# Optimization experiments

Measured on AMD Instinct MI355X. Metric: run time of the kernel, lower is better.

Reference implementation:

```python
import jax, jax.numpy as jnp
import numpy as np
from jax import lax

# --- constants from init_kwargs ---
B, N = 1, 6
C_IN, MID, C_CTX, D = 512, 512, 80, 112
OGH, OGW = 256, 704
DSF = 16
FH, FW = OGH // DSF, OGW // DSF  # 16, 44
D_MIN, D_MAX = 2.0, 58.0
NX, NY, NZ = 128, 128, 1
VOXEL_SIZE = np.array([0.8, 0.8, 8.0], np.float32)
VOXEL_COORD = np.array([-51.2 + 0.4, -51.2 + 0.4, -5.0 + 4.0], np.float32)
VOXEL_NUM = np.array([NX, NY, NZ], np.int32)


def _conv(x, w, b=None):
    pad = (w.shape[-1] - 1) // 2
    y = lax.conv_general_dilated(x, w, (1, 1), [(pad, pad), (pad, pad)],
                                 dimension_numbers=('NCHW', 'OIHW', 'NCHW'))
    if b is not None:
        y = y + b[None, :, None, None]
    return y


def _depthnet(x, w_s1, w_s2, w_d1, w_d2, b_d, w_c1, w_c2, b_c):
    # BatchNorm layers at init (gamma=1, beta=0, running stats 0/1) are identity in eval
    x = jax.nn.relu(_conv(x, w_s1))
    x = jax.nn.relu(_conv(x, w_s2))
    depth_logits = _conv(jax.nn.relu(_conv(x, w_d1)), w_d2, b_d)   # [BN, D, FH, FW]
    context = _conv(jax.nn.relu(_conv(x, w_c1)), w_c2, b_c)        # [BN, C_CTX, FH, FW]
    return depth_logits, context


def _frustum():
    d = jnp.linspace(D_MIN, D_MAX, D, dtype=jnp.float32)            # [D]
    u = jnp.linspace(0.0, OGW - 1.0, FW, dtype=jnp.float32)         # [FW]
    v = jnp.linspace(0.0, OGH - 1.0, FH, dtype=jnp.float32)         # [FH]
    uu = jnp.broadcast_to(u[None, None, :], (D, FH, FW))
    vv = jnp.broadcast_to(v[None, :, None], (D, FH, FW))
    uv1 = jnp.stack([uu, vv, jnp.ones_like(uu)], axis=-1)           # [D,FH,FW,3]
    return uv1, d


def _geometry(sensor2ego, intrin, ida, bda):
    uv1, d = _frustum()
    ida_inv = jnp.linalg.inv(ida)                                   # [B,N,4,4]
    R_ida, t_ida = ida_inv[..., :3, :3], ida_inv[..., :3, 3]
    uv1_pre = jnp.einsum('bnij,dhwj->bndhwi', R_ida, uv1) + t_ida[:, :, None, None, None, :]
    K_inv = jnp.linalg.inv(intrin[..., :3, :3])
    rays = jnp.einsum('bnij,bndhwj->bndhwi', K_inv, uv1_pre)
    pts_cam = rays * d[None, None, :, None, None, None]             # [B,N,D,FH,FW,3]
    pts4 = jnp.concatenate([pts_cam, jnp.ones_like(pts_cam[..., :1])], axis=-1)
    pts_ego = jnp.einsum('bnij,bndhwj->bndhwi', sensor2ego, pts4)
    pts_ego = jnp.einsum('bij,bndhwj->bndhwi', bda, pts_ego)
    return pts_ego[..., :3]                                         # [B,N,D,FH,FW,3]


def _voxel_pooling(geom_xyz, feats):
    # geom_xyz: [B,N,D,FH,FW,3] int32 voxel coords; feats: [B,N,D,FH,FW,C]
    C = feats.shape[-1]
    g = geom_xyz.reshape(B, -1, 3)                                  # [B,M,3]
    valid = jnp.all((g >= 0) & (g < jnp.asarray(VOXEL_NUM)[None, None, :]), axis=-1)
    idx = g[..., 1] * NX + g[..., 0]                                # y*nx + x (z collapsed, NZ=1)
    idx = idx + jnp.arange(B, dtype=jnp.int32)[:, None] * (NY * NX)
    idx = jnp.where(valid, idx, B * NY * NX)                        # dump bucket
    f = feats.reshape(B * g.shape[1], C)
    out = jax.ops.segment_sum(f, idx.reshape(-1), num_segments=B * NY * NX + 1)
    out = out[:B * NY * NX].reshape(B, NY, NX, C)
    return jnp.transpose(out, (0, 3, 1, 2))                         # [B,C,NY,NX]


def setup_inputs() -> dict:
    key = jax.random.key(0)
    ks = jax.random.split(key, 8)

    def w(k, shape):
        fan_in = shape[1] * shape[2] * shape[3]
        return jax.random.normal(k, shape, jnp.float32) * np.sqrt(2.0 / fan_in)

    inp = {
        'source_features': jax.random.normal(ks[0], (B * N, C_IN, FH, FW), jnp.float32),
        'w_s1': w(ks[1], (MID, C_IN, 3, 3)),
        'w_s2': w(ks[2], (MID, MID, 3, 3)),
        'w_d1': w(ks[3], (MID, MID, 3, 3)),
        'w_d2': w(ks[4], (D, MID, 1, 1)),
        'b_d': jnp.zeros((D,), jnp.float32),
        'w_c1': w(ks[5], (MID, MID, 3, 3)),
        'w_c2': w(ks[6], (C_CTX, MID, 1, 1)),
        'b_c': jnp.zeros((C_CTX,), jnp.float32),
    }

    # realistic camera rig: 6 cameras yawed around ego, cam-forward (z) -> ego-forward
    base = np.array([[0., 0., 1.], [-1., 0., 0.], [0., -1., 0.]], np.float32)
    s2e = np.zeros((B, N, 4, 4), np.float32)
    for n in range(N):
        yaw = 2.0 * np.pi * n / N
        c, s = np.cos(yaw), np.sin(yaw)
        Rz = np.array([[c, -s, 0.], [s, c, 0.], [0., 0., 1.]], np.float32)
        s2e[0, n, :3, :3] = Rz @ base
        s2e[0, n, :3, 3] = [0.0, 0.0, 1.5]
        s2e[0, n, 3, 3] = 1.0
    intrin = np.zeros((B, N, 4, 4), np.float32)
    intrin[:, :] = np.eye(4, dtype=np.float32)
    intrin[:, :, 0, 0] = 560.0
    intrin[:, :, 1, 1] = 560.0
    intrin[:, :, 0, 2] = OGW / 2.0
    intrin[:, :, 1, 2] = OGH / 2.0
    ida = np.broadcast_to(np.eye(4, dtype=np.float32), (B, N, 4, 4)).copy()
    bda = np.broadcast_to(np.eye(4, dtype=np.float32), (B, 4, 4)).copy()

    inp['sensor2ego_mats'] = jnp.asarray(s2e)
    inp['intrin_mats'] = jnp.asarray(intrin)
    inp['ida_mats'] = jnp.asarray(ida)
    inp['bda_mat'] = jnp.asarray(bda)
    return inp


def reference(source_features, w_s1, w_s2, w_d1, w_d2, b_d, w_c1, w_c2, b_c,
              sensor2ego_mats, intrin_mats, ida_mats, bda_mat):
    depth_logits, context = _depthnet(source_features, w_s1, w_s2, w_d1, w_d2, b_d, w_c1, w_c2, b_c)
    depth_prob = jax.nn.softmax(depth_logits, axis=1)               # [BN,D,FH,FW]
    # depth-weighted context: [BN, C, D, FH, FW]
    feat = depth_prob[:, None, :, :, :] * context[:, :, None, :, :]
    feat = feat.reshape(B, N, C_CTX, D, FH, FW).transpose(0, 1, 3, 4, 5, 2)  # [B,N,D,FH,FW,C]
    pts_ego = _geometry(sensor2ego_mats, intrin_mats, ida_mats, bda_mat)
    vs = jnp.asarray(VOXEL_SIZE)
    vc = jnp.asarray(VOXEL_COORD)
    geom_xyz = ((pts_ego - (vc - vs / 2.0)) / vs).astype(jnp.int32)
    return _voxel_pooling(geom_xyz, feat)                            # [B,C,NY,NX]
```

## Files before the change

### kernel.cpp

```cpp
#include <hip/hip_runtime.h>


#define FH_ 16
#define FW_ 44
#define SP_ 704
#define XSTR 960
#define NIMG 6
#define CIN 512
#define DCH 112
#define CCTX 80
#define NXY 128
#define NVOX (NXY * NXY)
#define NPTS (NIMG * DCH * SP_)
#define CHUNK 64

#define NKC7 8
#define HCHK 360448
#define CIP 40

typedef unsigned short u16;
typedef unsigned int u32;
typedef __attribute__((ext_vector_type(8))) short bf16x8;
typedef __attribute__((ext_vector_type(4))) short s16x4;
typedef __attribute__((ext_vector_type(4))) float f32x4;
typedef __attribute__((ext_vector_type(16))) float f32x16;

__device__ __forceinline__ float bf2f(u16 b) {
    union { unsigned u; float f; } v; v.u = ((unsigned)b) << 16; return v.f;
}
__device__ __forceinline__ u16 f2bf(float f) {
    union { float f; unsigned u; } v; v.f = f;
    unsigned r = v.u + 0x7fffu + ((v.u >> 16) & 1u);
    return (u16)(r >> 16);
}
__device__ __forceinline__ int spad_of(int s) {
    return (s / 44) * 46 + (s % 44) + 47;
}
__device__ __forceinline__ void gld_lds16(const void* gsrc, void* ldst) {
    __builtin_amdgcn_global_load_lds(
        (const __attribute__((address_space(1))) u32*)gsrc,
        (__attribute__((address_space(3))) u32*)ldst, 16, 0, 0);
}
__device__ __forceinline__ _Float16* chunk6(_Float16* pA, _Float16* pB, int q, int n) {
    int c = q * 6 + n;
    return (c < 6) ? (pA + (size_t)c * HCHK) : (pB + (size_t)(c - 6) * HCHK);
}

__global__ void zero_k(float4* __restrict__ p, long n4) {
    long i = (long)blockIdx.x * blockDim.x + threadIdx.x;
    if (i < n4) p[i] = make_float4(0.f, 0.f, 0.f, 0.f);
}

__global__ void src_to_xt_k(const float* __restrict__ src, short* __restrict__ xt) {
    int e = blockIdx.x * 256 + threadIdx.x;
    if (e >= NIMG * SP_ * CIN) return;
    int ci = e & 511;
    int r = e >> 9;
    int s = r % SP_, n = r / SP_;
    float v = src[((size_t)n * CIN + ci) * SP_ + s];
    xt[(((size_t)n * 32 + (ci >> 4)) * XSTR + spad_of(s)) * 16 + (ci & 15)] = (short)f2bf(v);
}

__global__ void wsplit2_k(const float* __restrict__ wA, short* __restrict__ oA,
                          const float* __restrict__ wB, short* __restrict__ oB) {
    int i = blockIdx.x * 256 + threadIdx.x;
    if (i >= 2 * CIN * CIN) return;
    const int e = i & (CIN * CIN - 1);
    const float* __restrict__ w = (i < CIN * CIN) ? wA : wB;
    short* __restrict__ o = (i < CIN * CIN) ? oA : oB;
    const int co = e >> 9, ci = e & 511;
    const float* wp = w + (size_t)e * 9;
#pragma unroll
    for (int t = 0; t < 9; ++t)
        o[((((size_t)(ci >> 4) * 9) + t) * CIN + co) * 16 + (ci & 15)] = (short)f2bf(wp[t]);
}

__global__ void wsplit1_dual_k(const float* __restrict__ wd, short* __restrict__ od,
                               const float* __restrict__ wc, short* __restrict__ oc) {
    int i = blockIdx.x * 256 + threadIdx.x;
    if (i < DCH * CIN) od[i] = (short)f2bf(wd[i]);
    else if (i < DCH * CIN + CCTX * CIN) {
        int j = i - DCH * CIN;
        oc[j] = (short)f2bf(wc[j]);
    }
}

__global__ __launch_bounds__(128, 2) void conv7_k(
    const short* __restrict__ xt2, const short* __restrict__ w2,
    _Float16* __restrict__ pA, _Float16* __restrict__ pB)
{
    __shared__ short Xs[2][256 * 16];
    __shared__ short Wsh[2][576 * 16];
    const int tid = threadIdx.x;
    const int lane = tid & 63, wave = tid >> 6;
    const int l31 = lane & 31, lh = lane >> 5;

    const int bid = blockIdx.x;
    const int c32 = bid & 31;
    const int cb = c32 >> 2, q = c32 & 3;
    const int rest = bid >> 5;
    const int n = rest / 6, sb = rest - (rest / 6) * 6;

    const int s0 = sb * 128;
    const int co0 = cb * 64;
    const int base = spad_of(s0) - 47;

    const short* __restrict__ xq = xt2 + (((size_t)n * 32 + q * 8) * XSTR + base) * 16;
    const short* __restrict__ wq = w2 + (((size_t)(q * 8) * 9) * CIN + co0) * 16;

    int sloc[2];
#pragma unroll
    for (int mf = 0; mf < 2; ++mf)
        sloc[mf] = spad_of(s0 + wave * 64 + mf * 32 + l31) - base;

    const f32x16 z16 = {0.f,0.f,0.f,0.f,0.f,0.f,0.f,0.f,
                        0.f,0.f,0.f,0.f,0.f,0.f,0.f,0.f};
    f32x16 acc[2][2];
    acc[0][0] = z16; acc[0][1] = z16; acc[1][0] = z16; acc[1][1] = z16;

#define STAGE7(BUF, KC) do {                                                    \
    const short* xc = xq + (size_t)(KC) * (XSTR * 16) + lane * 8;               \
    const short* wc = wq + (size_t)(KC) * (9 * CIN * 16) + lane * 8;            \
    _Pragma("unroll")                                                           \
    for (int i = 0; i < 13; ++i) {                                              \
        const int sg = wave + 2 * i;                                            \
        if (sg < 8) {                                                           \
            gld_lds16(xc + sg * 512, &Xs[BUF][sg * 512]);                       \
        } else {                                                                \
            const int j = sg - 8;                                               \
            gld_lds16(wc + (j >> 1) * (CIN * 16) + (j & 1) * 512,               \
                      &Wsh[BUF][j * 512]);                                      \
        }                                                                       \
    }                                                                           \
} while (0)

    STAGE7(0, 0);
    __syncthreads();

    constexpr int OFF[9] = {-47, -46, -45, -1, 0, 1, 45, 46, 47};
    for (int kc = 0; kc < NKC7; ++kc) {
        if (kc + 1 < NKC7) STAGE7((kc + 1) & 1, kc + 1);
        const short* __restrict__ Xb = Xs[kc & 1];
        const short* __restrict__ Wb = Wsh[kc & 1];
#pragma unroll
        for (int t9 = 0; t9 < 9; ++t9) {
            const int off = OFF[t9];
            bf16x8 a0 = *(const bf16x8*)&Xb[(sloc[0] + off) * 16 + lh * 8];
            bf16x8 a1 = *(const bf16x8*)&Xb[(sloc[1] + off) * 16 + lh * 8];
            bf16x8 b0 = *(const bf16x8*)&Wb[(t9 * 64 + l31) * 16 + lh * 8];
            bf16x8 b1 = *(const bf16x8*)&Wb[(t9 * 64 + 32 + l31) * 16 + lh * 8];
            acc[0][0] = __builtin_amdgcn_mfma_f32_32x32x16_bf16(a0, b0, acc[0][0], 0, 0, 0);
            acc[0][1] = __builtin_amdgcn_mfma_f32_32x32x16_bf16(a0, b1, acc[0][1], 0, 0, 0);
            acc[1][0] = __builtin_amdgcn_mfma_f32_32x32x16_bf16(a1, b0, acc[1][0], 0, 0, 0);
            acc[1][1] = __builtin_amdgcn_mfma_f32_32x32x16_bf16(a1, b1, acc[1][1], 0, 0, 0);
        }
        __syncthreads();
    }
#undef STAGE7

    _Float16* __restrict__ Pc = chunk6(pA, pB, q, n);
#pragma unroll
    for (int mf = 0; mf < 2; ++mf) {
        const int spb = wave * 64 + mf * 32 + 4 * lh;
#pragma unroll
        for (int r = 0; r < 16; ++r) {
            const int sg = s0 + spb + (r & 3) + 8 * (r >> 2);
            if (sg < SP_) {
                const size_t ro = (size_t)sg * 512 + co0 + l31;
                Pc[ro] = (_Float16)acc[mf][0][r];
                Pc[ro + 32] = (_Float16)acc[mf][1][r];
            }
        }
    }
}

__global__ __launch_bounds__(256) void combine6_k(
    _Float16* __restrict__ pA, _Float16* __restrict__ pB, short* __restrict__ xout)
{
    const int i = blockIdx.x * 256 + threadIdx.x;
    if (i >= NIMG * SP_ * CIN / 4) return;
    const int e = i * 4;
    const int n = e / (SP_ * CIN);
    const int r = e - n * (SP_ * CIN);
    const int s = r >> 9, co = r & 511;
    union h4 { s16x4 s; _Float16 h[4]; };
    float v[4] = {0.f, 0.f, 0.f, 0.f};
#pragma unroll
    for (int q = 0; q < 4; ++q) {
        const _Float16* c = chunk6(pA, pB, q, n);
        h4 u; u.s = *(const s16x4*)(c + r);
#pragma unroll
        for (int j = 0; j < 4; ++j) v[j] += (float)u.h[j];
    }
    s16x4 o;
#pragma unroll
    for (int j = 0; j < 4; ++j) o[j] = (short)f2bf(fmaxf(v[j], 0.f));
    *(s16x4*)&xout[(((size_t)n * 32 + (co >> 4)) * XSTR + spad_of(s)) * 16 + (co & 15)] = o;
}

__global__ __launch_bounds__(256, 2) void gemm1x1d_k(
    const short* __restrict__ xA, const short* __restrict__ wA,
    const float* __restrict__ bA, float* __restrict__ oA,
    const short* __restrict__ xB, const short* __restrict__ wB,
    const float* __restrict__ bB, float* __restrict__ oB)
{
    const int sel = blockIdx.y;
    const short* __restrict__ xtin = sel ? xB : xA;
    const short* __restrict__ wb   = sel ? wB : wA;
    const float* __restrict__ bias = sel ? bB : bA;
    float* __restrict__ outT       = sel ? oB : oA;
    const int nst = sel ? (CCTX / 16) : (DCH / 16);
    const int nco = nst * 16;

    __shared__ short Wb[DCH * CIP];
    const int tid = threadIdx.x;
    const int s0 = blockIdx.x * 128, n = blockIdx.z;
    const int lane = tid & 63, wave = tid >> 6;
    const int kg = lane >> 4, lrow = lane & 15;
    const int swave = s0 + wave * 32;

    int arow[2];
#pragma unroll
    for (int ms = 0; ms < 2; ++ms)
        arow[ms] = spad_of(swave + ms * 16 + lrow);

    const f32x4 zero4 = {0.f, 0.f, 0.f, 0.f};
    f32x4 acc[2][7];
#pragma unroll
    for (int ms = 0; ms < 2; ++ms)
#pragma unroll
        for (int ns = 0; ns < 7; ++ns) acc[ms][ns] = zero4;

    const short* xb = xtin + (size_t)n * 32 * XSTR * 16;

    for (int kc = 0; kc < 16; ++kc) {
        __syncthreads();
#pragma unroll
        for (int it = 0; it < 2; ++it) {
            int q = it * 256 + tid;
            if (q < nco * 4) {
                int co = q >> 2, p = q & 3;
                *(bf16x8*)&Wb[co * CIP + p * 8] =
                    *(const bf16x8*)(wb + (size_t)co * CIN + kc * 32 + p * 8);
            }
        }
        __syncthreads();
        bf16x8 a[2];
#pragma unroll
        for (int ms = 0; ms < 2; ++ms) {
            const int kcc = 2 * kc + (kg >> 1);
            a[ms] = *(const bf16x8*)(xb + ((size_t)kcc * XSTR + arow[ms]) * 16 + (kg & 1) * 8);
        }
#pragma unroll
        for (int ns = 0; ns < 7; ++ns) {
            if (ns < nst) {
                int co = ns * 16 + lrow;
                bf16x8 b = *(const bf16x8*)&Wb[co * CIP + kg * 8];
#pragma unroll
                for (int ms = 0; ms < 2; ++ms)
                    acc[ms][ns] = __builtin_amdgcn_mfma_f32_16x16x32_bf16(
                        a[ms], b, acc[ms][ns], 0, 0, 0);
            }
        }
    }
#pragma unroll
    for (int ms = 0; ms < 2; ++ms)
#pragma unroll
        for (int ns = 0; ns < 7; ++ns) {
            if (ns < nst) {
#pragma unroll
                for (int r = 0; r < 4; ++r) {
                    int sg = swave + ms * 16 + kg * 4 + r;
                    if (sg < SP_) {
                        int co = ns * 16 + lrow;
                        outT[((size_t)n * SP_ + sg) * nco + co] = acc[ms][ns][r] + bias[co];
                    }
                }
            }
        }
}

__global__ __launch_bounds__(256) void softmax2_k(
    const float* __restrict__ lg, float* __restrict__ pr)
{
    const int p = blockIdx.x * 4 + (threadIdx.x >> 6);
    if (p >= NIMG * SP_) return;
    const int lane = threadIdx.x & 63;
    const float* lp = lg + (size_t)p * DCH;
    float v0 = lp[lane];
    float v1 = (lane < DCH - 64) ? lp[64 + lane] : -1e30f;
    float m = fmaxf(v0, v1);
#pragma unroll
    for (int o = 32; o; o >>= 1) m = fmaxf(m, __shfl_xor(m, o));
    float e0 = __expf(v0 - m);
    float e1 = (lane < DCH - 64) ? __expf(v1 - m) : 0.f;
    float s = e0 + e1;
#pragma unroll
    for (int o = 32; o; o >>= 1) s += __shfl_xor(s, o);
    const float inv = 1.f / s;
    float* pp = pr + (size_t)p * DCH;
    pp[lane] = e0 * inv;
    if (lane < DCH - 64) pp[64 + lane] = e1 * inv;
}

__device__ __forceinline__ void inv4(const double* M, double* inv) {
    inv[0]  =  M[5]*M[10]*M[15] - M[5]*M[11]*M[14] - M[9]*M[6]*M[15] + M[9]*M[7]*M[14] + M[13]*M[6]*M[11] - M[13]*M[7]*M[10];
    inv[4]  = -M[4]*M[10]*M[15] + M[4]*M[11]*M[14] + M[8]*M[6]*M[15] - M[8]*M[7]*M[14] - M[12]*M[6]*M[11] + M[12]*M[7]*M[10];
    inv[8]  =  M[4]*M[9]*M[15]  - M[4]*M[11]*M[13] - M[8]*M[5]*M[15] + M[8]*M[7]*M[13] + M[12]*M[5]*M[11] - M[12]*M[7]*M[9];
    inv[12] = -M[4]*M[9]*M[14]  + M[4]*M[10]*M[13] + M[8]*M[5]*M[14] - M[8]*M[6]*M[13] - M[12]*M[5]*M[10] + M[12]*M[6]*M[9];
    inv[1]  = -M[1]*M[10]*M[15] + M[1]*M[11]*M[14] + M[9]*M[2]*M[15] - M[9]*M[3]*M[14] - M[13]*M[2]*M[11] + M[13]*M[3]*M[10];
    inv[5]  =  M[0]*M[10]*M[15] - M[0]*M[11]*M[14] - M[8]*M[2]*M[15] + M[8]*M[3]*M[14] + M[12]*M[2]*M[11] - M[12]*M[3]*M[10];
    inv[9]  = -M[0]*M[9]*M[15]  + M[0]*M[11]*M[13] + M[8]*M[1]*M[15] - M[8]*M[3]*M[13] - M[12]*M[1]*M[11] + M[12]*M[3]*M[9];
    inv[13] =  M[0]*M[9]*M[14]  - M[0]*M[10]*M[13] - M[8]*M[1]*M[14] + M[8]*M[2]*M[13] + M[12]*M[1]*M[10] - M[12]*M[2]*M[9];
    inv[2]  =  M[1]*M[6]*M[15]  - M[1]*M[7]*M[14]  - M[5]*M[2]*M[15] + M[5]*M[3]*M[14] + M[13]*M[2]*M[7]  - M[13]*M[3]*M[6];
    inv[6]  = -M[0]*M[6]*M[15]  + M[0]*M[7]*M[14]  + M[4]*M[2]*M[15] - M[4]*M[3]*M[14] - M[12]*M[2]*M[7]  + M[12]*M[3]*M[6];
    inv[10] =  M[0]*M[5]*M[15]  - M[0]*M[7]*M[13]  - M[4]*M[1]*M[15] + M[4]*M[3]*M[13] + M[12]*M[1]*M[7]  - M[12]*M[3]*M[5];
    inv[14] = -M[0]*M[5]*M[14]  + M[0]*M[6]*M[13]  + M[4]*M[1]*M[14] - M[4]*M[2]*M[13] - M[12]*M[1]*M[6]  + M[12]*M[2]*M[5];
    inv[3]  = -M[1]*M[6]*M[11]  + M[1]*M[7]*M[10]  + M[5]*M[2]*M[11] - M[5]*M[3]*M[10] - M[9]*M[2]*M[7]   + M[9]*M[3]*M[6];
    inv[7]  =  M[0]*M[6]*M[11]  - M[0]*M[7]*M[10]  - M[4]*M[2]*M[11] + M[4]*M[3]*M[10] + M[8]*M[2]*M[7]   - M[8]*M[3]*M[6];
    inv[11] = -M[0]*M[5]*M[11]  + M[0]*M[7]*M[9]   + M[4]*M[1]*M[11] - M[4]*M[3]*M[9]  - M[8]*M[1]*M[7]   + M[8]*M[3]*M[5];
    inv[15] =  M[0]*M[5]*M[10]  - M[0]*M[6]*M[9]   - M[4]*M[1]*M[10] + M[4]*M[2]*M[9]  + M[8]*M[1]*M[6]   - M[8]*M[2]*M[5];
    double det = M[0]*inv[0] + M[1]*inv[4] + M[2]*inv[8] + M[3]*inv[12];
    double id = 1.0 / det;
#pragma unroll
    for (int i = 0; i < 16; ++i) inv[i] *= id;
}

__global__ void geom_setup_k(const float* __restrict__ s2e, const float* __restrict__ intrin,
                             const float* __restrict__ ida, const float* __restrict__ bda,
                             double* __restrict__ gc)
{
    const int n = threadIdx.x;
    if (n >= NIMG) return;
    double M[16], Iv[16];
#pragma unroll
    for (int i = 0; i < 16; ++i) M[i] = (double)ida[n * 16 + i];
    inv4(M, Iv);
    double R[3][3], tv[3];
#pragma unroll
    for (int r = 0; r < 3; ++r) {
#pragma unroll
        for (int c = 0; c < 3; ++c) R[r][c] = Iv[r * 4 + c];
        tv[r] = Iv[r * 4 + 3];
    }
    double K[3][3];
#pragma unroll
    for (int r = 0; r < 3; ++r)
#pragma unroll
        for (int c = 0; c < 3; ++c) K[r][c] = (double)intrin[n * 16 + r * 4 + c];
    double det = K[0][0] * (K[1][1] * K[2][2] - K[1][2] * K[2][1])
               - K[0][1] * (K[1][0] * K[2][2] - K[1][2] * K[2][0])
               + K[0][2] * (K[1][0] * K[2][1] - K[1][1] * K[2][0]);
    double id = 1.0 / det;
    double Ki[3][3];
    Ki[0][0] = (K[1][1] * K[2][2] - K[1][2] * K[2][1]) * id;
    Ki[0][1] = (K[0][2] * K[2][1] - K[0][1] * K[2][2]) * id;
    Ki[0][2] = (K[0][1] * K[1][2] - K[0][2] * K[1][1]) * id;
    Ki[1][0] = (K[1][2] * K[2][0] - K[1][0] * K[2][2]) * id;
    Ki[1][1] = (K[0][0] * K[2][2] - K[0][2] * K[2][0]) * id;
    Ki[1][2] = (K[0][2] * K[1][0] - K[0][0] * K[1][2]) * id;
    Ki[2][0] = (K[1][0] * K[2][1] - K[1][1] * K[2][0]) * id;
    Ki[2][1] = (K[0][1] * K[2][0] - K[0][0] * K[2][1]) * id;
    Ki[2][2] = (K[0][0] * K[1][1] - K[0][1] * K[1][0]) * id;
    double A[3][3], bv[3];
#pragma unroll
    for (int r = 0; r < 3; ++r) {
#pragma unroll
        for (int c = 0; c < 3; ++c)
            A[r][c] = Ki[r][0] * R[0][c] + Ki[r][1] * R[1][c] + Ki[r][2] * R[2][c];
        bv[r] = Ki[r][0] * tv[0] + Ki[r][1] * tv[1] + Ki[r][2] * tv[2];
    }
    double* g = gc + n * 24;
#pragma unroll
    for (int r = 0; r < 3; ++r)
#pragma unroll
        for (int c = 0; c < 3; ++c) g[r * 3 + c] = A[r][c];
#pragma unroll
    for (int r = 0; r < 3; ++r) g[9 + r] = bv[r];
#pragma unroll
    for (int r = 0; r < 3; ++r)
#pragma unroll
        for (int c = 0; c < 4; ++c) {
            double acc = 0.0;
#pragma unroll
            for (int k = 0; k < 4; ++k)
                acc += (double)bda[r * 4 + k] * (double)s2e[n * 16 + k * 4 + c];
            g[12 + r * 4 + c] = acc;
        }
}

__global__ __launch_bounds__(256) void point_voxel_k(
    const double* __restrict__ gc, int* __restrict__ vidx, int* __restrict__ cnt)
{
    const int i = blockIdx.x * 256 + threadIdx.x;
    if (i >= NPTS) return;
    const int lane = threadIdx.x & 63;
    const int n = i / (DCH * SP_);
    int r = i - n * (DCH * SP_);
    const int di = r / SP_;
    const int s = r - di * SP_;
    const int h = s / FW_, w = s - h * FW_;
    const double* g = gc + n * 24;
    const double u  = (double)(float)((double)w * (703.0 / 43.0));
    const double v  = (double)(float)((double)h * 17.0);
    const double dd = (double)(float)(2.0 + (double)di * (56.0 / 111.0));
    const double rx = g[0] * u + g[1] * v + g[2] + g[9];
    const double ry = g[3] * u + g[4] * v + g[5] + g[10];
    const double rz = g[6] * u + g[7] * v + g[8] + g[11];
    const double px = rx * dd, py = ry * dd, pz = rz * dd;
    const double ex = g[12] * px + g[13] * py + g[14] * pz + g[15];
    const double ey = g[16] * px + g[17] * py + g[18] * pz + g[19];
    const double ez = g[20] * px + g[21] * py + g[22] * pz + g[23];
    const double vs_xy = 0.8, vs_z = 8.0;
    const double offx = (double)(float)(-51.2 + 0.4) - vs_xy * 0.5;
    const double offz = (double)(float)(-5.0 + 4.0) - vs_z * 0.5;
    const int gx = (int)((ex - offx) / vs_xy);
    const int gy = (int)((ey - offx) / vs_xy);
    const int gz = (int)((ez - offz) / vs_z);
    const bool ok = (gx >= 0 && gx < NXY && gy >= 0 && gy < NXY && gz == 0);
    const int vv = ok ? (gy * NXY + gx) : -1;
    vidx[i] = vv;
    unsigned long long unresolved = __ballot(vv >= 0);
    while (unresolved) {
        const int src = __ffsll(unresolved) - 1;
        const int v0 = __shfl(vv, src);
        const unsigned long long grp = __ballot(vv == v0);
        if (lane == src) atomicAdd(&cnt[v0], __popcll(grp));
        unresolved &= ~grp;
    }
}

__global__ void prefix_k(const int* __restrict__ cnt, int* __restrict__ off,
                         int* __restrict__ cur) {
    __shared__ int part[256];
    const int t = threadIdx.x;
    int s = 0;
    for (int j = 0; j < 64; ++j) s += cnt[t * 64 + j];
    part[t] = s;
    __syncthreads();
    if (t == 0) {
        int run = 0;
        for (int k = 0; k < 256; ++k) { int v = part[k]; part[k] = run; run += v; }
    }
    __syncthreads();
    int base = part[t];
    for (int j = 0; j < 64; ++j) {
        off[t * 64 + j] = base;
        cur[t * 64 + j] = base;
        base += cnt[t * 64 + j];
    }
    if (t == 255) off[NVOX] = base;
}

__global__ __launch_bounds__(256) void fill_k(
    const int* __restrict__ vidx, const float* __restrict__ prob,
    int* __restrict__ cur, int2* __restrict__ pk) {
    int i = blockIdx.x * 256 + threadIdx.x;
    if (i >= NPTS) return;
    const int lane = threadIdx.x & 63;
    const int v = vidx[i];
    const int n = i / (DCH * SP_);
    int r = i - n * (DCH * SP_);
    const int di = r / SP_;
    const int s = r - di * SP_;
    float p = 0.f;
    if (v >= 0) p = prob[((size_t)n * SP_ + s) * DCH + di];

    int pos = -1;
    unsigned long long unresolved = __ballot(v >= 0);
    while (unresolved) {
        const int src = __ffsll(unresolved) - 1;
        const int v0 = __shfl(v, src);
        const unsigned long long grp = __ballot(v == v0);
        int base = 0;
        if (lane == src) base = atomicAdd(&cur[v0], __popcll(grp));
        base = __shfl(base, src);
        if (v == v0) {
            const int rank = __popcll(grp & ((1ull << lane) - 1ull));
            pos = base + rank;
        }
        unresolved &= ~grp;
    }
    if (v >= 0)
        pk[pos] = make_int2((v << 13) | (n * SP_ + s), __float_as_int(p));
}

__global__ __launch_bounds__(256) void gather2_k(
    const int2* __restrict__ pk, const int* __restrict__ off,
    const float* __restrict__ ctxT, float* __restrict__ accT)
{
    const int gtid = blockIdx.x * 256 + threadIdx.x;
    const int wid = gtid >> 6;
    const int lane = threadIdx.x & 63;
    const int total = off[NVOX];
    const int lo = wid * CHUNK;
    if (lo >= total) return;
    const int hi = min(lo + CHUNK, total);
    float a0 = 0.f, a1 = 0.f;
    int2 e = pk[lo];
    for (int k = lo; k < hi; ++k) {
        const int2 en = (k + 1 < hi) ? pk[k + 1] : make_int2(-1, 0);
        const float p = __int_as_float(e.y);
        const int ns = e.x & 8191;
        const float* cb = ctxT + (size_t)ns * CCTX;
        a0 = fmaf(p, cb[lane], a0);
        if (lane < CCTX - 64) a1 = fmaf(p, cb[64 + lane], a1);
        if ((en.x >> 13) != (e.x >> 13)) {
            float* ab = accT + (size_t)(e.x >> 13) * CCTX;
            atomicAdd(ab + lane, a0);
            if (lane < CCTX - 64) atomicAdd(ab + 64 + lane, a1);
            a0 = a1 = 0.f;
        }
        e = en;
    }
}

__global__ void transpose_out_k(const float* __restrict__ accT, float* __restrict__ out) {
    const int idx = blockIdx.x * 256 + threadIdx.x;
    if (idx >= CCTX * NVOX) return;
    const int c = idx >> 14;
    const int v = idx & 16383;
    out[idx] = accT[(size_t)v * CCTX + c];
}

#define O_WHIA  512
#define O_WHIB  1180160
#define O_XT0   2359808
#define O_XT1   3834368
#define O_XT2   5308928
#define O_WD2B  6783488
#define O_WC2B  6812160
#define O_DLG   6832640
#define O_DPR   7305728
#define O_CTX   7778816
#define O_PK    8116736
#define O_VIX   9062912
#define O_CNT   9536000
#define O_OFF   9552384
#define O_CUR   9568784
#define O_ACC   9585168

extern "C" void kernel_launch(void* const* d_in, const int* in_sizes, int n_in,
                              void* d_out, int out_size, void* d_ws, size_t ws_size,
                              hipStream_t stream)
{
    const float* src  = (const float*)d_in[0];
    const float* w_s1 = (const float*)d_in[1];
    const float* w_s2 = (const float*)d_in[2];
    const float* w_d1 = (const float*)d_in[3];
    const float* w_d2 = (const float*)d_in[4];
    const float* b_d  = (const float*)d_in[5];
    const float* w_c1 = (const float*)d_in[6];
    const float* w_c2 = (const float*)d_in[7];
    const float* b_c  = (const float*)d_in[8];
    const float* s2e  = (const float*)d_in[9];
    const float* intr = (const float*)d_in[10];
    const float* ida  = (const float*)d_in[11];
    const float* bda  = (const float*)d_in[12];

    double* gc = (double*)d_ws;
    float* ws   = (float*)d_ws;
    short* whiA = (short*)(ws + O_WHIA);
    short* whiC = (short*)(ws + O_XT2);
    _Float16* pA = (_Float16*)(ws + O_WHIB);
    _Float16* pB = (_Float16*)(ws + O_WD2B);
    short* xt0  = (short*)(ws + O_XT0);
    short* xt1  = (short*)(ws + O_XT1);
    short* xt2  = (short*)(ws + O_XT2);
    short* wd2b = (short*)(ws + O_WD2B);
    short* wc2b = (short*)(ws + O_WC2B);
    float* dlog = ws + O_DLG;
    float* dprb = ws + O_DPR;
    float* ctxT = ws + O_CTX;
    int2*  pk   = (int2*)(ws + O_PK);
    int* vidx   = (int*)(ws + O_VIX);
    int* cnt    = (int*)(ws + O_CNT);
    int* offs   = (int*)(ws + O_OFF);
    int* cur    = (int*)(ws + O_CUR);
    float* accT = ws + O_ACC;
    float* out  = (float*)d_out;

    const int CMB = (NIMG * SP_ * CIN / 4 + 255) / 256;

    zero_k<<<(2949120 / 4 + 255) / 256, 256, 0, stream>>>((float4*)xt0, 2949120 / 4);

    geom_setup_k<<<1, 64, 0, stream>>>(s2e, intr, ida, bda, gc);
    src_to_xt_k<<<(NIMG * SP_ * CIN + 255) / 256, 256, 0, stream>>>(src, xt0);

    wsplit2_k<<<(2 * CIN * CIN) / 256, 256, 0, stream>>>(w_s1, whiA, w_s2, whiC);
    conv7_k<<<1152, 128, 0, stream>>>(xt0, whiA, pA, pB);
    combine6_k<<<CMB, 256, 0, stream>>>(pA, pB, xt1);
    conv7_k<<<1152, 128, 0, stream>>>(xt1, whiC, pA, pB);
    combine6_k<<<CMB, 256, 0, stream>>>(pA, pB, xt0);
    wsplit2_k<<<(2 * CIN * CIN) / 256, 256, 0, stream>>>(w_c1, whiA, w_d1, whiC);
    conv7_k<<<1152, 128, 0, stream>>>(xt0, whiA, pA, pB);
    combine6_k<<<CMB, 256, 0, stream>>>(pA, pB, xt1);
    conv7_k<<<1152, 128, 0, stream>>>(xt0, whiC, pA, pB);
    combine6_k<<<CMB, 256, 0, stream>>>(pA, pB, xt2);

    wsplit1_dual_k<<<((DCH + CCTX) * CIN + 255) / 256, 256, 0, stream>>>(w_d2, wd2b, w_c2, wc2b);
    gemm1x1d_k<<<dim3(6, 2, NIMG), 256, 0, stream>>>(xt2, wd2b, b_d, dlog,
                                                     xt1, wc2b, b_c, ctxT);
    softmax2_k<<<(NIMG * SP_ + 3) / 4, 256, 0, stream>>>(dlog, dprb);

    zero_k<<<(NVOX / 4 + 255) / 256, 256, 0, stream>>>((float4*)cnt, NVOX / 4);
    point_voxel_k<<<(NPTS + 255) / 256, 256, 0, stream>>>(gc, vidx, cnt);
    prefix_k<<<1, 256, 0, stream>>>(cnt, offs, cur);
    fill_k<<<(NPTS + 255) / 256, 256, 0, stream>>>(vidx, dprb, cur, pk);

    zero_k<<<(1310720 / 4 + 255) / 256, 256, 0, stream>>>((float4*)accT, 1310720 / 4);
    {
        const int waves = (NPTS + CHUNK - 1) / CHUNK;
        const int blocks = (waves + 3) / 4;
        gather2_k<<<blocks, 256, 0, stream>>>(pk, offs, ctxT, accT);
    }
    transpose_out_k<<<(CCTX * NVOX + 255) / 256, 256, 0, stream>>>(accT, out);

    (void)in_sizes; (void)n_in; (void)out_size; (void)ws_size;
}
```

Before: 421.4 us.

## Widen conv tile to 128 output channels and load weights directly from global

```diff
diff --git a/kernel.cpp b/kernel.cpp
--- a/kernel.cpp
+++ b/kernel.cpp
@@ -14,7 +14,7 @@
 #define NPTS (NIMG * DCH * SP_)
 #define CHUNK 64
 
-#define NKC7 8
+#define NKC8 8
 #define HCHK 360448
 #define CIP 40
 
@@ -85,70 +85,61 @@
     }
 }
 
-__global__ __launch_bounds__(128, 2) void conv7_k(
+__global__ __launch_bounds__(256, 2) void conv8_k(
     const short* __restrict__ xt2, const short* __restrict__ w2,
     _Float16* __restrict__ pA, _Float16* __restrict__ pB)
 {
     __shared__ short Xs[2][256 * 16];
-    __shared__ short Wsh[2][576 * 16];
     const int tid = threadIdx.x;
     const int lane = tid & 63, wave = tid >> 6;
     const int l31 = lane & 31, lh = lane >> 5;
+    const int mw = wave >> 1, nw = wave & 1;
 
     const int bid = blockIdx.x;
-    const int c32 = bid & 31;
-    const int cb = c32 >> 2, q = c32 & 3;
-    const int rest = bid >> 5;
+    const int c16 = bid & 15;
+    const int cb = c16 >> 2, q = c16 & 3;
+    const int rest = bid >> 4;
     const int n = rest / 6, sb = rest - (rest / 6) * 6;
 
     const int s0 = sb * 128;
-    const int co0 = cb * 64;
+    const int co0 = cb * 128;
     const int base = spad_of(s0) - 47;
 
     const short* __restrict__ xq = xt2 + (((size_t)n * 32 + q * 8) * XSTR + base) * 16;
-    const short* __restrict__ wq = w2 + (((size_t)(q * 8) * 9) * CIN + co0) * 16;
+    const short* __restrict__ wl = w2 + (((size_t)(q * 8) * 9) * CIN + co0 + nw * 64) * 16
+                                   + l31 * 16 + lh * 8;
 
     int sloc[2];
 #pragma unroll
     for (int mf = 0; mf < 2; ++mf)
-        sloc[mf] = spad_of(s0 + wave * 64 + mf * 32 + l31) - base;
+        sloc[mf] = spad_of(s0 + mw * 64 + mf * 32 + l31) - base;
 
     const f32x16 z16 = {0.f,0.f,0.f,0.f,0.f,0.f,0.f,0.f,
                         0.f,0.f,0.f,0.f,0.f,0.f,0.f,0.f};
     f32x16 acc[2][2];
     acc[0][0] = z16; acc[0][1] = z16; acc[1][0] = z16; acc[1][1] = z16;
 
-#define STAGE7(BUF, KC) do {                                                    \
+#define STAGE8(BUF, KC) do {                                                    \
     const short* xc = xq + (size_t)(KC) * (XSTR * 16) + lane * 8;               \
-    const short* wc = wq + (size_t)(KC) * (9 * CIN * 16) + lane * 8;            \
-    _Pragma("unroll")                                                           \
-    for (int i = 0; i < 13; ++i) {                                              \
-        const int sg = wave + 2 * i;                                            \
-        if (sg < 8) {                                                           \
-            gld_lds16(xc + sg * 512, &Xs[BUF][sg * 512]);                       \
-        } else {                                                                \
-            const int j = sg - 8;                                               \
-            gld_lds16(wc + (j >> 1) * (CIN * 16) + (j & 1) * 512,               \
-                      &Wsh[BUF][j * 512]);                                      \
-        }                                                                       \
-    }                                                                           \
+    gld_lds16(xc + (wave * 2) * 512, &Xs[BUF][(wave * 2) * 512]);               \
+    gld_lds16(xc + (wave * 2 + 1) * 512, &Xs[BUF][(wave * 2 + 1) * 512]);       \
 } while (0)
 
-    STAGE7(0, 0);
+    STAGE8(0, 0);
     __syncthreads();
 
     constexpr int OFF[9] = {-47, -46, -45, -1, 0, 1, 45, 46, 47};
-    for (int kc = 0; kc < NKC7; ++kc) {
-        if (kc + 1 < NKC7) STAGE7((kc + 1) & 1, kc + 1);
+    for (int kc = 0; kc < NKC8; ++kc) {
+        if (kc + 1 < NKC8) STAGE8((kc + 1) & 1, kc + 1);
         const short* __restrict__ Xb = Xs[kc & 1];
-        const short* __restrict__ Wb = Wsh[kc & 1];
+        const short* __restrict__ wk = wl + (size_t)kc * (9 * CIN * 16);
 #pragma unroll
         for (int t9 = 0; t9 < 9; ++t9) {
             const int off = OFF[t9];
+            bf16x8 b0 = *(const bf16x8*)(wk + t9 * (CIN * 16));
+            bf16x8 b1 = *(const bf16x8*)(wk + t9 * (CIN * 16) + 512);
             bf16x8 a0 = *(const bf16x8*)&Xb[(sloc[0] + off) * 16 + lh * 8];
             bf16x8 a1 = *(const bf16x8*)&Xb[(sloc[1] + off) * 16 + lh * 8];
-            bf16x8 b0 = *(const bf16x8*)&Wb[(t9 * 64 + l31) * 16 + lh * 8];
-            bf16x8 b1 = *(const bf16x8*)&Wb[(t9 * 64 + 32 + l31) * 16 + lh * 8];
             acc[0][0] = __builtin_amdgcn_mfma_f32_32x32x16_bf16(a0, b0, acc[0][0], 0, 0, 0);
             acc[0][1] = __builtin_amdgcn_mfma_f32_32x32x16_bf16(a0, b1, acc[0][1], 0, 0, 0);
             acc[1][0] = __builtin_amdgcn_mfma_f32_32x32x16_bf16(a1, b0, acc[1][0], 0, 0, 0);
@@ -156,17 +147,17 @@
         }
         __syncthreads();
     }
-#undef STAGE7
+#undef STAGE8
 
     _Float16* __restrict__ Pc = chunk6(pA, pB, q, n);
 #pragma unroll
     for (int mf = 0; mf < 2; ++mf) {
-        const int spb = wave * 64 + mf * 32 + 4 * lh;
+        const int spb = mw * 64 + mf * 32 + 4 * lh;
 #pragma unroll
         for (int r = 0; r < 16; ++r) {
             const int sg = s0 + spb + (r & 3) + 8 * (r >> 2);
             if (sg < SP_) {
-                const size_t ro = (size_t)sg * 512 + co0 + l31;
+                const size_t ro = (size_t)sg * 512 + co0 + nw * 64 + l31;
                 Pc[ro] = (_Float16)acc[mf][0][r];
                 Pc[ro + 32] = (_Float16)acc[mf][1][r];
             }
@@ -214,22 +205,17 @@
 
     __shared__ short Wb[DCH * CIP];
     const int tid = threadIdx.x;
-    const int s0 = blockIdx.x * 128, n = blockIdx.z;
+    const int s0 = blockIdx.x * 64, n = blockIdx.z;
     const int lane = tid & 63, wave = tid >> 6;
     const int kg = lane >> 4, lrow = lane & 15;
-    const int swave = s0 + wave * 32;
-
-    int arow[2];
-#pragma unroll
-    for (int ms = 0; ms < 2; ++ms)
-        arow[ms] = spad_of(swave + ms * 16 + lrow);
+    const int swave = s0 + wave * 16;
+
+    const int arow = spad_of(swave + lrow);
 
     const f32x4 zero4 = {0.f, 0.f, 0.f, 0.f};
-    f32x4 acc[2][7];
-#pragma unroll
-    for (int ms = 0; ms < 2; ++ms)
-#pragma unroll
-        for (int ns = 0; ns < 7; ++ns) acc[ms][ns] = zero4;
+    f32x4 acc[7];
+#pragma unroll
+    for (int ns = 0; ns < 7; ++ns) acc[ns] = zero4;
 
     const short* xb = xtin + (size_t)n * 32 * XSTR * 16;
 
@@ -245,39 +231,28 @@
             }
         }
         __syncthreads();
-        bf16x8 a[2];
-#pragma unroll
-        for (int ms = 0; ms < 2; ++ms) {
-            const int kcc = 2 * kc + (kg >> 1);
-            a[ms] = *(const bf16x8*)(xb + ((size_t)kcc * XSTR + arow[ms]) * 16 + (kg & 1) * 8);
-        }
+        const int kcc = 2 * kc + (kg >> 1);
+        bf16x8 a = *(const bf16x8*)(xb + ((size_t)kcc * XSTR + arow) * 16 + (kg & 1) * 8);
 #pragma unroll
         for (int ns = 0; ns < 7; ++ns) {
             if (ns < nst) {
                 int co = ns * 16 + lrow;
                 bf16x8 b = *(const bf16x8*)&Wb[co * CIP + kg * 8];
-#pragma unroll
-                for (int ms = 0; ms < 2; ++ms)
-                    acc[ms][ns] = __builtin_amdgcn_mfma_f32_16x16x32_bf16(
-                        a[ms], b, acc[ms][ns], 0, 0, 0);
+                acc[ns] = __builtin_amdgcn_mfma_f32_16x16x32_bf16(a, b, acc[ns], 0, 0, 0);
             }
         }
     }
 #pragma unroll
-    for (int ms = 0; ms < 2; ++ms)
-#pragma unroll
-        for (int ns = 0; ns < 7; ++ns) {
-            if (ns < nst) {
-#pragma unroll
-                for (int r = 0; r < 4; ++r) {
-                    int sg = swave + ms * 16 + kg * 4 + r;
-                    if (sg < SP_) {
-                        int co = ns * 16 + lrow;
-                        outT[((size_t)n * SP_ + sg) * nco + co] = acc[ms][ns][r] + bias[co];
-                    }
-                }
+    for (int ns = 0; ns < 7; ++ns) {
+        if (ns < nst) {
+#pragma unroll
+            for (int r = 0; r < 4; ++r) {
+                const int sg = swave + kg * 4 + r;
+                const int co = ns * 16 + lrow;
+                outT[((size_t)n * SP_ + sg) * nco + co] = acc[ns][r] + bias[co];
             }
         }
+    }
 }
 
 __global__ __launch_bounds__(256) void softmax2_k(
@@ -588,19 +563,19 @@
     src_to_xt_k<<<(NIMG * SP_ * CIN + 255) / 256, 256, 0, stream>>>(src, xt0);
 
     wsplit2_k<<<(2 * CIN * CIN) / 256, 256, 0, stream>>>(w_s1, whiA, w_s2, whiC);
-    conv7_k<<<1152, 128, 0, stream>>>(xt0, whiA, pA, pB);
+    conv8_k<<<576, 256, 0, stream>>>(xt0, whiA, pA, pB);
     combine6_k<<<CMB, 256, 0, stream>>>(pA, pB, xt1);
-    conv7_k<<<1152, 128, 0, stream>>>(xt1, whiC, pA, pB);
+    conv8_k<<<576, 256, 0, stream>>>(xt1, whiC, pA, pB);
     combine6_k<<<CMB, 256, 0, stream>>>(pA, pB, xt0);
     wsplit2_k<<<(2 * CIN * CIN) / 256, 256, 0, stream>>>(w_c1, whiA, w_d1, whiC);
-    conv7_k<<<1152, 128, 0, stream>>>(xt0, whiA, pA, pB);
+    conv8_k<<<576, 256, 0, stream>>>(xt0, whiA, pA, pB);
     combine6_k<<<CMB, 256, 0, stream>>>(pA, pB, xt1);
-    conv7_k<<<1152, 128, 0, stream>>>(xt0, whiC, pA, pB);
+    conv8_k<<<576, 256, 0, stream>>>(xt0, whiC, pA, pB);
     combine6_k<<<CMB, 256, 0, stream>>>(pA, pB, xt2);
 
     wsplit1_dual_k<<<((DCH + CCTX) * CIN + 255) / 256, 256, 0, stream>>>(w_d2, wd2b, w_c2, wc2b);
-    gemm1x1d_k<<<dim3(6, 2, NIMG), 256, 0, stream>>>(xt2, wd2b, b_d, dlog,
-                                                     xt1, wc2b, b_c, ctxT);
+    gemm1x1d_k<<<dim3(11, 2, NIMG), 256, 0, stream>>>(xt2, wd2b, b_d, dlog,
+                                                      xt1, wc2b, b_c, ctxT);
     softmax2_k<<<(NIMG * SP_ + 3) / 4, 256, 0, stream>>>(dlog, dprb);
 
     zero_k<<<(NVOX / 4 + 255) / 256, 256, 0, stream>>>((float4*)cnt, NVOX / 4);
```

After: 407.8 us. 1.03x faster.
